# Optimization experiments

Hardware: AMD Instinct MI355X
Metric: run time of the kernel (lower is better)

The kernel has to match this reference:

```python
import jax, jax.numpy as jnp
import numpy as np

N = 5000      # nodes per event (hardcoded in PFNet7.forward)
BIN = 100     # LSH bin_size
K = 16        # kNN per node within bin
SLOPE = 0.01  # LeakyReLU default negative slope


def _mlp(x, W1, b1, W2, b2, W3, b3):
    h = jax.nn.leaky_relu(x @ W1 + b1, SLOPE)
    h = jax.nn.leaky_relu(h @ W2 + b2, SLOPE)
    return h @ W3 + b3


def _build_graph_lsh(x, codebook):
    # x: [N, F]. Faithful vectorized version of GraphBuildingLSH (batch=1).
    n_bins = N // BIN                                   # 50
    mul = x @ codebook[:, : n_bins // 2]                # [N, 25]
    cmul = jnp.concatenate([mul, -mul], axis=-1)        # [N, 50]
    bin_idx = jnp.argmax(cmul, axis=-1)                 # [N]
    bins_split = jnp.argsort(bin_idx).reshape(n_bins, BIN)  # [nb, BIN]
    pts = x[bins_split]                                 # [nb, BIN, F]
    dm = jax.nn.sigmoid(jnp.einsum('pif,pjf->pij', pts, pts))  # [nb, BIN, BIN]
    vals, inds = jax.lax.top_k(dm, K)                   # [nb, BIN, K]
    src = jnp.broadcast_to(bins_split[:, :, None], inds.shape).reshape(-1)
    dst = jnp.take_along_axis(bins_split, inds.reshape(n_bins, -1), axis=1).reshape(-1)
    val = vals.reshape(-1)                              # [nb*BIN*K] = 80000 edges
    return src, dst, val


def _gcn_conv(x, W, b, src, dst, ew):
    # PyG GCNConv: add self-loops (weight 1), symmetric normalization, aggregate at col.
    n = x.shape[0]
    loop = jnp.arange(n)
    row = jnp.concatenate([src, loop])
    col = jnp.concatenate([dst, loop])
    w = jnp.concatenate([ew, jnp.ones((n,), x.dtype)])
    deg = jax.ops.segment_sum(w, col, num_segments=n)
    dis = jnp.where(deg > 0, deg ** -0.5, 0.0)
    norm = dis[row] * w * dis[col]
    h = x @ W
    out = jax.ops.segment_sum(norm[:, None] * h[row], col, num_segments=n)
    return out + b


def _graph_conv(x, Wrel, brel, Wroot, src, dst, ew):
    # PyG GraphConv(aggr='add'): lin_rel(sum_j w_ij x_j) + lin_root(x)
    agg = jax.ops.segment_sum(ew[:, None] * x[src], dst, num_segments=x.shape[0])
    return agg @ Wrel + brel + x @ Wroot


def setup_inputs() -> dict:
    key = jax.random.key(0)
    ks = jax.random.split(key, 24)
    f32 = jnp.float32
    d = {
        'x': jax.random.normal(ks[0], (N, 12), f32),
        'ygen_id': jax.random.normal(ks[1], (N, 6), f32),
        'ygen': jax.random.normal(ks[2], (N, 6), f32),
        'codebook': jax.random.normal(ks[3], (12, 100), f32),
        # nn1: 12 -> 125 -> 125 -> 12
        'nn1_W1': jax.random.normal(ks[4], (12, 125), f32) * 0.1,
        'nn1_b1': jnp.zeros((125,), f32),
        'nn1_W2': jax.random.normal(ks[5], (125, 125), f32) * 0.1,
        'nn1_b2': jnp.zeros((125,), f32),
        'nn1_W3': jax.random.normal(ks[6], (125, 12), f32) * 0.1,
        'nn1_b3': jnp.zeros((12,), f32),
        # GCNConv: 12 -> 32
        'gcn_W': jax.random.normal(ks[7], (12, 32), f32) * 0.1,
        'gcn_b': jnp.zeros((32,), f32),
        # GraphConv: 32 -> 32
        'gc_Wrel': jax.random.normal(ks[8], (32, 32), f32) * 0.1,
        'gc_brel': jnp.zeros((32,), f32),
        'gc_Wroot': jax.random.normal(ks[9], (32, 32), f32) * 0.1,
        # nn2: 32 -> 125 -> 125 -> 6
        'nn2_W1': jax.random.normal(ks[10], (32, 125), f32) * 0.1,
        'nn2_b1': jnp.zeros((125,), f32),
        'nn2_W2': jax.random.normal(ks[11], (125, 125), f32) * 0.1,
        'nn2_b2': jnp.zeros((125,), f32),
        'nn2_W3': jax.random.normal(ks[12], (125, 6), f32) * 0.1,
        'nn2_b3': jnp.zeros((6,), f32),
        # nn3: 38 -> 125 -> 125 -> 6
        'nn3_W1': jax.random.normal(ks[13], (38, 125), f32) * 0.1,
        'nn3_b1': jnp.zeros((125,), f32),
        'nn3_W2': jax.random.normal(ks[14], (125, 125), f32) * 0.1,
        'nn3_b2': jnp.zeros((125,), f32),
        'nn3_W3': jax.random.normal(ks[15], (125, 6), f32) * 0.1,
        'nn3_b3': jnp.zeros((6,), f32),
    }
    return d


def reference(x, ygen_id, ygen, codebook,
              nn1_W1, nn1_b1, nn1_W2, nn1_b2, nn1_W3, nn1_b3,
              gcn_W, gcn_b, gc_Wrel, gc_brel, gc_Wroot,
              nn2_W1, nn2_b1, nn2_W2, nn2_b2, nn2_W3, nn2_b3,
              nn3_W1, nn3_b1, nn3_W2, nn3_b2, nn3_W3, nn3_b3):
    h = _mlp(x, nn1_W1, nn1_b1, nn1_W2, nn1_b2, nn1_W3, nn1_b3)   # [N, 12]
    src, dst, ew = _build_graph_lsh(h, codebook)
    h = jax.nn.leaky_relu(h, SLOPE)
    h = _gcn_conv(h, gcn_W, gcn_b, src, dst, ew)                   # [N, 32]
    h = _graph_conv(h, gc_Wrel, gc_brel, gc_Wroot, src, dst, ew)
    h = jax.nn.leaky_relu(h, SLOPE)
    cand_ids = _mlp(h, nn2_W1, nn2_b1, nn2_W2, nn2_b2, nn2_W3, nn2_b3)
    cand_p4 = _mlp(jnp.concatenate([h, cand_ids], axis=-1),
                   nn3_W1, nn3_b1, nn3_W2, nn3_b2, nn3_W3, nn3_b3)
    return (cand_ids, cand_p4, ygen_id, ygen)
```

## Files before the change

kernel.cpp:

```cpp
#include <hip/hip_runtime.h>
#include <math.h>

#define NN 5000
#define NBINS 50
#define BINSZ 100
#define KNN 16
#define BPAD 104
#define NB 20

typedef _Float16 half8 __attribute__((ext_vector_type(8)));

__device__ __forceinline__ float lrelu(float x){ return x >= 0.f ? x : 0.01f*x; }

__device__ __forceinline__ void scatter_w(float* dst, int t, float4 v) {
    int e = 4 * t, r = e / 125, c = e - 125 * r;
    dst[r * 128 + c] = v.x; if (++c == 125) { c = 0; ++r; }
    dst[r * 128 + c] = v.y; if (++c == 125) { c = 0; ++r; }
    dst[r * 128 + c] = v.z; if (++c == 125) { c = 0; ++r; }
    dst[r * 128 + c] = v.w;
}

__global__ __launch_bounds__(640) void nn1_kernel(
    const float* __restrict__ x,
    const float* __restrict__ W1, const float* __restrict__ b1,
    const float* __restrict__ W2, const float* __restrict__ b2,
    const float* __restrict__ W3, const float* __restrict__ b3,
    const float* __restrict__ cb,
    float* __restrict__ h_out, int* __restrict__ bin_idx) {
    __shared__ float sW[8192];
    __shared__ float bufX[12 * NB];
    __shared__ float bufA[125 * NB];
    __shared__ float bufB[125 * NB];
    __shared__ float sCB[300];
    int tid = threadIdx.x;
    int n0 = blockIdx.x * NB;
    int g = tid >> 7, j = tid & 127;
    float acc[4];
    float4 r0, r1; float rt = 0.f;

    if (tid < 60) {
        float4 v = ((const float4*)(x + n0 * 12))[tid];
        int e = tid * 4;
        bufX[(e % 12) * NB + (e / 12)] = v.x;
        bufX[((e + 1) % 12) * NB + ((e + 1) / 12)] = v.y;
        bufX[((e + 2) % 12) * NB + ((e + 2) / 12)] = v.z;
        bufX[((e + 3) % 12) * NB + ((e + 3) / 12)] = v.w;
    }
    if (tid < 300) { int k = tid / 25, c = tid - k * 25; sCB[tid] = cb[k * 100 + c]; }
    if (tid < 375) ((float4*)sW)[tid] = ((const float4*)W1)[tid];
    __syncthreads();

    if (j < 125) {
        float bj = b1[j];
        acc[0] = bj; acc[1] = bj; acc[2] = bj; acc[3] = bj;
        #pragma unroll
        for (int k = 0; k < 12; ++k) {
            float w = sW[k * 125 + j];
            float4 a = *(const float4*)&bufX[k * NB + g * 4];
            acc[0] += a.x * w; acc[1] += a.y * w; acc[2] += a.z * w; acc[3] += a.w * w;
        }
        #pragma unroll
        for (int n = 0; n < 4; ++n) bufA[j * NB + g * 4 + n] = lrelu(acc[n]);
    }
    r0 = (tid < 1000) ? ((const float4*)W2)[tid] : make_float4(0.f,0.f,0.f,0.f);
    r1 = (tid < 360)  ? ((const float4*)W2)[tid + 640] : make_float4(0.f,0.f,0.f,0.f);
    __syncthreads();
    if (tid < 1000) scatter_w(sW, tid, r0);
    if (tid < 360)  scatter_w(sW, tid + 640, r1);
    __syncthreads();

    float acc8[8];
    if (tid < 320) {
        int j4 = tid & 31;
        #pragma unroll
        for (int jj = 0; jj < 4; ++jj) {
            int jc = 4 * j4 + jj;
            float bj = (jc < 125) ? b2[jc] : 0.f;
            acc8[2 * jj] = bj; acc8[2 * jj + 1] = bj;
        }
    }
    for (int c = 0; c < 4; ++c) {
        if (c < 3) {
            int base = (c + 1) * 1000, nf4 = (c + 1 < 3) ? 1000 : 906;
            r0 = (tid < nf4) ? ((const float4*)W2)[base + tid] : make_float4(0.f,0.f,0.f,0.f);
            r1 = (tid + 640 < nf4) ? ((const float4*)W2)[base + tid + 640] : make_float4(0.f,0.f,0.f,0.f);
            if (c + 1 == 3 && tid == 0) rt = W2[15624];
        }
        int nk = (c < 3) ? 32 : 29;
        if (tid < 320) {
            int j4 = tid & 31, n2 = tid >> 5;
            const float* wbuf = sW + (c & 1) * 4096;
            const float* arow = bufA + (c * 32) * NB + 2 * n2;
            for (int k = 0; k < nk; ++k) {
                float4 w4 = *(const float4*)&wbuf[k * 128 + 4 * j4];
                float2 a2 = *(const float2*)&arow[k * NB];
                acc8[0] += w4.x * a2.x; acc8[1] += w4.x * a2.y;
                acc8[2] += w4.y * a2.x; acc8[3] += w4.y * a2.y;
                acc8[4] += w4.z * a2.x; acc8[5] += w4.z * a2.y;
                acc8[6] += w4.w * a2.x; acc8[7] += w4.w * a2.y;
            }
        }
        if (c < 3) {
            float* dst = sW + ((c + 1) & 1) * 4096;
            int nf4 = (c + 1 < 3) ? 1000 : 906;
            if (tid < nf4) scatter_w(dst, tid, r0);
            if (tid + 640 < nf4) scatter_w(dst, tid + 640, r1);
            if (c + 1 == 3 && tid == 0) dst[3708] = rt;
            __syncthreads();
        }
    }
    if (tid < 320) {
        int j4 = tid & 31, n2 = tid >> 5;
        #pragma unroll
        for (int jj = 0; jj < 4; ++jj) {
            int jc = 4 * j4 + jj;
            if (jc < 125) {
                bufB[jc * NB + 2 * n2]     = lrelu(acc8[2 * jj]);
                bufB[jc * NB + 2 * n2 + 1] = lrelu(acc8[2 * jj + 1]);
            }
        }
    }
    __syncthreads();
    if (tid < 375) ((float4*)sW)[tid] = ((const float4*)W3)[tid];
    __syncthreads();

    if (j < 48) {
        int jj = j % 12, s = j / 12;
        int k0 = s * 32, nk = (s < 3) ? 32 : 29;
        float ps[4] = {0.f, 0.f, 0.f, 0.f};
        for (int k = 0; k < nk; ++k) {
            float w = sW[(k0 + k) * 12 + jj];
            float4 a = *(const float4*)&bufB[(k0 + k) * NB + g * 4];
            ps[0] += a.x * w; ps[1] += a.y * w; ps[2] += a.z * w; ps[3] += a.w * w;
        }
        #pragma unroll
        for (int n = 0; n < 4; ++n) bufA[(s * 12 + jj) * NB + g * 4 + n] = ps[n];
    }
    __syncthreads();
    if (tid < 240) {
        int jj = tid / 20, n = tid % 20;
        float v = bufA[jj * NB + n] + bufA[(12 + jj) * NB + n]
                + bufA[(24 + jj) * NB + n] + bufA[(36 + jj) * NB + n] + b3[jj];
        h_out[(n0 + n) * 12 + jj] = v;
        bufB[jj * NB + n] = v;
    }
    __syncthreads();

    if (tid < NB) {
        int n = tid;
        float hv[12];
        #pragma unroll
        for (int k = 0; k < 12; ++k) hv[k] = bufB[k * NB + n];
        float best = -INFINITY; int bi = 0;
        for (int c = 0; c < 25; ++c) {
            float m = 0.f;
            #pragma unroll
            for (int k = 0; k < 12; ++k) m += hv[k] * sCB[k * 25 + c];
            if (m > best) { best = m; bi = c; }
        }
        for (int c = 0; c < 25; ++c) {
            float m = 0.f;
            #pragma unroll
            for (int k = 0; k < 12; ++k) m += hv[k] * sCB[k * 25 + c];
            if (-m > best) { best = -m; bi = c + 25; }
        }
        bin_idx[n0 + n] = bi;
    }
}

__global__ __launch_bounds__(64) void scatter_kernel(
    const int* __restrict__ bin_idx, int* __restrict__ order) {
    __shared__ int sBI[NN];
    int b = blockIdx.x, lane = threadIdx.x;
    for (int t = lane; t < NN / 4; t += 64) ((int4*)sBI)[t] = ((const int4*)bin_idx)[t];
    __syncthreads();
    unsigned long long below = (lane == 0) ? 0ULL : ((~0ULL) >> (64 - lane));
    int cnt_lt = 0;
    for (int base = 0; base < NN; base += 64) {
        int i = base + lane;
        int bi = (i < NN) ? sBI[i] : 999;
        cnt_lt += __popcll(__ballot(bi < b));
    }
    int offs = cnt_lt;
    for (int base = 0; base < NN; base += 64) {
        int i = base + lane;
        int bi = (i < NN) ? sBI[i] : 999;
        unsigned long long m = __ballot(bi == b);
        if (bi == b) order[offs + __popcll(m & below)] = i;
        offs += __popcll(m);
    }
}

__global__ __launch_bounds__(640) void graph2_kernel(
    const float* __restrict__ h, const int* __restrict__ order,
    const float* __restrict__ gcn_W, const float* __restrict__ gcn_b,
    float* __restrict__ gcn_n, float* __restrict__ agg_n,
    const float4* __restrict__ ygen_id4, const float4* __restrict__ ygen4,
    float4* __restrict__ out4) {
    __shared__ _Float16 M[BINSZ * BPAD];
    __shared__ float s_h[BINSZ * 12];
    __shared__ int   s_nodes[BINSZ];
    __shared__ float s_dis[BINSZ];
    __shared__ float s_w[12 * 32];
    __shared__ float s_big[2 * 32 * BPAD];
    float* s_hWd = s_big;
    float* s_gcn = s_big + 32 * BPAD;
    unsigned* s_tv = (unsigned*)s_big;
    int p = blockIdx.x, tid = threadIdx.x;

    if (tid < BINSZ) s_nodes[tid] = order[p * BINSZ + tid];
    for (int t = tid; t < BINSZ * BPAD / 2; t += 640) ((int*)M)[t] = 0;
    if (tid < 384) s_w[tid] = gcn_W[tid];
    if (tid < 300) {
        int gI = p * 300 + tid;
        out4[15000 + gI] = (gI < 7500) ? ygen_id4[gI] : ygen4[gI - 7500];
    }
    __syncthreads();
    for (int t = tid; t < BINSZ * 12; t += 640) {
        int i = t / 12, k = t - i * 12;
        s_h[t] = h[s_nodes[i] * 12 + k];
    }
    __syncthreads();

    if (tid < 200) {
        int row = tid >> 1, half = tid & 1;
        const float4* xp = (const float4*)&s_h[row * 12];
        float4 x0 = xp[0], x1 = xp[1], x2 = xp[2];
        unsigned tv[KNN];
        #pragma unroll
        for (int k = 0; k < KNN; ++k) tv[k] = 0u;
        int j0 = half * 50;
        for (int jj = 0; jj < 50; ++jj) {
            int j = j0 + jj;
            const float4* ap = (const float4*)&s_h[j * 12];
            float4 a0 = ap[0], a1 = ap[1], a2 = ap[2];
            float d = x0.x*a0.x + x0.y*a0.y + x0.z*a0.z + x0.w*a0.w
                    + x1.x*a1.x + x1.y*a1.y + x1.z*a1.z + x1.w*a1.w
                    + x2.x*a2.x + x2.y*a2.y + x2.z*a2.z + x2.w*a2.w;
            float v = 1.f / (1.f + expf(-d));
            unsigned key = (__float_as_uint(v) & 0xFFFFFF80u) | (unsigned)(127 - j);
            if (key > tv[KNN - 1]) {
                unsigned ins = key;
                #pragma unroll
                for (int k = 0; k < KNN; ++k) {
                    bool gt = ins > tv[k];
                    unsigned mx = gt ? ins : tv[k];
                    unsigned mn = gt ? tv[k] : ins;
                    tv[k] = mx; ins = mn;
                }
            }
        }
        #pragma unroll
        for (int k = 0; k < KNN; ++k) s_tv[tid * KNN + k] = tv[k];
    }
    __syncthreads();

    if (tid < BINSZ) {
        int base = tid * 32;
        int ia = 0, ib = 0;
        #pragma unroll
        for (int k = 0; k < KNN; ++k) {
            unsigned av = s_tv[base + ia], bv = s_tv[base + 16 + ib];
            bool tA = av > bv;
            unsigned key = tA ? av : bv;
            ia += tA; ib += !tA;
            int ix = 127 - (int)(key & 127u);
            float v = __uint_as_float(key & 0xFFFFFF80u);
            M[ix * BPAD + tid] = (_Float16)v;
        }
    }
    __syncthreads();

    if (tid < BINSZ) {
        float dsum = 1.0f;
        #pragma unroll 13
        for (int sc = 0; sc < 13; ++sc) {
            half8 m = *(const half8*)&M[tid * BPAD + sc * 8];
            dsum += (float)m[0] + (float)m[1] + (float)m[2] + (float)m[3]
                  + (float)m[4] + (float)m[5] + (float)m[6] + (float)m[7];
        }
        s_dis[tid] = 1.0f / sqrtf(dsum);
    }
    __syncthreads();

    for (int o = tid; o < BINSZ * 32; o += 640) {
        int s = o >> 5, cc = o & 31;
        float a = 0.f;
        #pragma unroll
        for (int k = 0; k < 12; ++k) a += lrelu(s_h[s * 12 + k]) * s_w[k * 32 + cc];
        s_hWd[cc * BPAD + s] = s_dis[s] * a;
    }
    if (tid < 128) {
        s_hWd[(tid >> 2) * BPAD + 100 + (tid & 3)] = 0.f;
        s_gcn[(tid >> 2) * BPAD + 100 + (tid & 3)] = 0.f;
    }
    __syncthreads();

    int cc = tid & 31, dgg = tid >> 5;
    {
        float a5[5] = {0.f, 0.f, 0.f, 0.f, 0.f};
        for (int sc = 0; sc < 13; ++sc) {
            float4 hv0 = *(const float4*)&s_hWd[cc * BPAD + sc * 8];
            float4 hv1 = *(const float4*)&s_hWd[cc * BPAD + sc * 8 + 4];
            #pragma unroll
            for (int r = 0; r < 5; ++r) {
                int d = dgg + 20 * r;
                half8 m = *(const half8*)&M[d * BPAD + sc * 8];
                a5[r] += (float)m[0]*hv0.x + (float)m[1]*hv0.y + (float)m[2]*hv0.z + (float)m[3]*hv0.w
                       + (float)m[4]*hv1.x + (float)m[5]*hv1.y + (float)m[6]*hv1.z + (float)m[7]*hv1.w;
            }
        }
        float bc = gcn_b[cc];
        #pragma unroll
        for (int r = 0; r < 5; ++r) {
            int d = dgg + 20 * r;
            float gq = s_dis[d] * (a5[r] + s_hWd[cc * BPAD + d]) + bc;
            s_gcn[cc * BPAD + d] = gq;
            gcn_n[s_nodes[d] * 32 + cc] = gq;
        }
    }
    __syncthreads();
    {
        float a5[5] = {0.f, 0.f, 0.f, 0.f, 0.f};
        for (int sc = 0; sc < 13; ++sc) {
            float4 hv0 = *(const float4*)&s_gcn[cc * BPAD + sc * 8];
            float4 hv1 = *(const float4*)&s_gcn[cc * BPAD + sc * 8 + 4];
            #pragma unroll
            for (int r = 0; r < 5; ++r) {
                int d = dgg + 20 * r;
                half8 m = *(const half8*)&M[d * BPAD + sc * 8];
                a5[r] += (float)m[0]*hv0.x + (float)m[1]*hv0.y + (float)m[2]*hv0.z + (float)m[3]*hv0.w
                       + (float)m[4]*hv1.x + (float)m[5]*hv1.y + (float)m[6]*hv1.z + (float)m[7]*hv1.w;
            }
        }
        #pragma unroll
        for (int r = 0; r < 5; ++r) {
            int d = dgg + 20 * r;
            agg_n[s_nodes[d] * 32 + cc] = a5[r];
        }
    }
}

__global__ __launch_bounds__(640) void nn23_kernel(
    const float* __restrict__ gcn_n, const float* __restrict__ agg_n,
    const float* __restrict__ Wrel, const float* __restrict__ brel,
    const float* __restrict__ Wroot,
    const float* __restrict__ A1, const float* __restrict__ ab1,
    const float* __restrict__ A2, const float* __restrict__ ab2,
    const float* __restrict__ A3, const float* __restrict__ ab3,
    const float* __restrict__ B1, const float* __restrict__ bb1,
    const float* __restrict__ B2, const float* __restrict__ bb2,
    const float* __restrict__ B3, const float* __restrict__ bb3,
    float* __restrict__ out_ids, float* __restrict__ out_p4) {
    __shared__ float sW[8192];
    __shared__ float sAG[32 * NB];
    __shared__ float sGC[32 * NB];
    __shared__ float bufC[38 * NB];
    __shared__ float bufA[125 * NB];
    __shared__ float bufB[125 * NB];
    int tid = threadIdx.x;
    int n0 = blockIdx.x * NB;
    int g = tid >> 7, j = tid & 127;
    float acc[4];
    float acc8[8];
    float4 r0, r1; float rt = 0.f;

    if (tid < 160) {
        float4 va = ((const float4*)(agg_n + n0 * 32))[tid];
        float4 vg = ((const float4*)(gcn_n + n0 * 32))[tid];
        int e = tid * 4, n = e / 32, k = e % 32;
        sAG[k * NB + n] = va.x; sAG[(k+1) * NB + n] = va.y;
        sAG[(k+2) * NB + n] = va.z; sAG[(k+3) * NB + n] = va.w;
        sGC[k * NB + n] = vg.x; sGC[(k+1) * NB + n] = vg.y;
        sGC[(k+2) * NB + n] = vg.z; sGC[(k+3) * NB + n] = vg.w;
    }
    if (tid >= 160 && tid < 416) ((float4*)sW)[tid - 160] = ((const float4*)Wrel)[tid - 160];
    if (tid >= 416 && tid < 640) ((float4*)(sW + 1024))[tid - 416] = ((const float4*)Wroot)[tid - 416];
    if (tid < 32) ((float4*)(sW + 1024))[224 + tid] = ((const float4*)Wroot)[224 + tid];
    for (int t = tid; t < 1000; t += 640) ((float4*)(sW + 2048))[t] = ((const float4*)A1)[t];
    __syncthreads();

    {
        int jc = tid / 20, n = tid % 20;
        float a = brel[jc];
        #pragma unroll 8
        for (int k = 0; k < 32; ++k)
            a += sAG[k * NB + n] * sW[k * 32 + jc] + sGC[k * NB + n] * sW[1024 + k * 32 + jc];
        bufC[jc * NB + n] = lrelu(a);
    }
    __syncthreads();

    if (j < 125) {
        float bj = ab1[j];
        acc[0] = bj; acc[1] = bj; acc[2] = bj; acc[3] = bj;
        #pragma unroll 8
        for (int k = 0; k < 32; ++k) {
            float w = sW[2048 + k * 125 + j];
            float4 a = *(const float4*)&bufC[k * NB + g * 4];
            acc[0] += a.x * w; acc[1] += a.y * w; acc[2] += a.z * w; acc[3] += a.w * w;
        }
        #pragma unroll
        for (int n = 0; n < 4; ++n) bufA[j * NB + g * 4 + n] = lrelu(acc[n]);
    }
    r0 = (tid < 1000) ? ((const float4*)A2)[tid] : make_float4(0.f,0.f,0.f,0.f);
    r1 = (tid < 360)  ? ((const float4*)A2)[tid + 640] : make_float4(0.f,0.f,0.f,0.f);
    __syncthreads();
    if (tid < 1000) scatter_w(sW, tid, r0);
    if (tid < 360)  scatter_w(sW, tid + 640, r1);
    __syncthreads();

    if (tid < 320) {
        int j4 = tid & 31;
        #pragma unroll
        for (int jj = 0; jj < 4; ++jj) {
            int jc = 4 * j4 + jj;
            float bj = (jc < 125) ? ab2[jc] : 0.f;
            acc8[2 * jj] = bj; acc8[2 * jj + 1] = bj;
        }
    }
    for (int c = 0; c < 4; ++c) {
        if (c < 3) {
            int base = (c + 1) * 1000, nf4 = (c + 1 < 3) ? 1000 : 906;
            r0 = (tid < nf4) ? ((const float4*)A2)[base + tid] : make_float4(0.f,0.f,0.f,0.f);
            r1 = (tid + 640 < nf4) ? ((const float4*)A2)[base + tid + 640] : make_float4(0.f,0.f,0.f,0.f);
            if (c + 1 == 3 && tid == 0) rt = A2[15624];
        }
        int nk = (c < 3) ? 32 : 29;
        if (tid < 320) {
            int j4 = tid & 31, n2 = tid >> 5;
            const float* wbuf = sW + (c & 1) * 4096;
            const float* arow = bufA + (c * 32) * NB + 2 * n2;
            for (int k = 0; k < nk; ++k) {
                float4 w4 = *(const float4*)&wbuf[k * 128 + 4 * j4];
                float2 a2 = *(const float2*)&arow[k * NB];
                acc8[0] += w4.x * a2.x; acc8[1] += w4.x * a2.y;
                acc8[2] += w4.y * a2.x; acc8[3] += w4.y * a2.y;
                acc8[4] += w4.z * a2.x; acc8[5] += w4.z * a2.y;
                acc8[6] += w4.w * a2.x; acc8[7] += w4.w * a2.y;
            }
        }
        if (c < 3) {
            float* dst = sW + ((c + 1) & 1) * 4096;
            int nf4 = (c + 1 < 3) ? 1000 : 906;
            if (tid < nf4) scatter_w(dst, tid, r0);
            if (tid + 640 < nf4) scatter_w(dst, tid + 640, r1);
            if (c + 1 == 3 && tid == 0) dst[3708] = rt;
            __syncthreads();
        }
    }
    if (tid < 320) {
        int j4 = tid & 31, n2 = tid >> 5;
        #pragma unroll
        for (int jj = 0; jj < 4; ++jj) {
            int jc = 4 * j4 + jj;
            if (jc < 125) {
                bufB[jc * NB + 2 * n2]     = lrelu(acc8[2 * jj]);
                bufB[jc * NB + 2 * n2 + 1] = lrelu(acc8[2 * jj + 1]);
            }
        }
    }
    __syncthreads();
    if (tid < 187) ((float4*)sW)[tid] = ((const float4*)A3)[tid];
    if (tid == 187) { sW[748] = A3[748]; sW[749] = A3[749]; }
    for (int t = tid; t < 1187; t += 640) ((float4*)(sW + 752))[t] = ((const float4*)B1)[t];
    if (tid == 188) { sW[752 + 4748] = B1[4748]; sW[752 + 4749] = B1[4749]; }
    __syncthreads();

    if (j < 24) {
        int jj = j % 6, s = j / 6;
        int k0 = s * 32, nk = (s < 3) ? 32 : 29;
        float ps[4] = {0.f, 0.f, 0.f, 0.f};
        for (int k = 0; k < nk; ++k) {
            float w = sW[(k0 + k) * 6 + jj];
            float4 a = *(const float4*)&bufB[(k0 + k) * NB + g * 4];
            ps[0] += a.x * w; ps[1] += a.y * w; ps[2] += a.z * w; ps[3] += a.w * w;
        }
        #pragma unroll
        for (int n = 0; n < 4; ++n) bufA[(s * 6 + jj) * NB + g * 4 + n] = ps[n];
    }
    __syncthreads();
    if (tid < 120) {
        int jj = tid / 20, n = tid % 20;
        float v = bufA[jj * NB + n] + bufA[(6 + jj) * NB + n]
                + bufA[(12 + jj) * NB + n] + bufA[(18 + jj) * NB + n] + ab3[jj];
        out_ids[(n0 + n) * 6 + jj] = v;
        bufC[(32 + jj) * NB + n] = v;
    }
    __syncthreads();

    if (j < 125) {
        float bj = bb1[j];
        acc[0] = bj; acc[1] = bj; acc[2] = bj; acc[3] = bj;
        #pragma unroll 2
        for (int k = 0; k < 38; ++k) {
            float w = sW[752 + k * 125 + j];
            float4 a = *(const float4*)&bufC[k * NB + g * 4];
            acc[0] += a.x * w; acc[1] += a.y * w; acc[2] += a.z * w; acc[3] += a.w * w;
        }
        #pragma unroll
        for (int n = 0; n < 4; ++n) bufA[j * NB + g * 4 + n] = lrelu(acc[n]);
    }
    r0 = (tid < 1000) ? ((const float4*)B2)[tid] : make_float4(0.f,0.f,0.f,0.f);
    r1 = (tid < 360)  ? ((const float4*)B2)[tid + 640] : make_float4(0.f,0.f,0.f,0.f);
    __syncthreads();
    if (tid < 1000) scatter_w(sW, tid, r0);
    if (tid < 360)  scatter_w(sW, tid + 640, r1);
    __syncthreads();

    if (tid < 320) {
        int j4 = tid & 31;
        #pragma unroll
        for (int jj = 0; jj < 4; ++jj) {
            int jc = 4 * j4 + jj;
            float bj = (jc < 125) ? bb2[jc] : 0.f;
            acc8[2 * jj] = bj; acc8[2 * jj + 1] = bj;
        }
    }
    for (int c = 0; c < 4; ++c) {
        if (c < 3) {
            int base = (c + 1) * 1000, nf4 = (c + 1 < 3) ? 1000 : 906;
            r0 = (tid < nf4) ? ((const float4*)B2)[base + tid] : make_float4(0.f,0.f,0.f,0.f);
            r1 = (tid + 640 < nf4) ? ((const float4*)B2)[base + tid + 640] : make_float4(0.f,0.f,0.f,0.f);
            if (c + 1 == 3 && tid == 0) rt = B2[15624];
        }
        int nk = (c < 3) ? 32 : 29;
        if (tid < 320) {
            int j4 = tid & 31, n2 = tid >> 5;
            const float* wbuf = sW + (c & 1) * 4096;
            const float* arow = bufA + (c * 32) * NB + 2 * n2;
            for (int k = 0; k < nk; ++k) {
                float4 w4 = *(const float4*)&wbuf[k * 128 + 4 * j4];
                float2 a2 = *(const float2*)&arow[k * NB];
                acc8[0] += w4.x * a2.x; acc8[1] += w4.x * a2.y;
                acc8[2] += w4.y * a2.x; acc8[3] += w4.y * a2.y;
                acc8[4] += w4.z * a2.x; acc8[5] += w4.z * a2.y;
                acc8[6] += w4.w * a2.x; acc8[7] += w4.w * a2.y;
            }
        }
        if (c < 3) {
            float* dst = sW + ((c + 1) & 1) * 4096;
            int nf4 = (c + 1 < 3) ? 1000 : 906;
            if (tid < nf4) scatter_w(dst, tid, r0);
            if (tid + 640 < nf4) scatter_w(dst, tid + 640, r1);
            if (c + 1 == 3 && tid == 0) dst[3708] = rt;
            __syncthreads();
        }
    }
    if (tid < 320) {
        int j4 = tid & 31, n2 = tid >> 5;
        #pragma unroll
        for (int jj = 0; jj < 4; ++jj) {
            int jc = 4 * j4 + jj;
            if (jc < 125) {
                bufB[jc * NB + 2 * n2]     = lrelu(acc8[2 * jj]);
                bufB[jc * NB + 2 * n2 + 1] = lrelu(acc8[2 * jj + 1]);
            }
        }
    }
    __syncthreads();
    if (tid < 187) ((float4*)sW)[tid] = ((const float4*)B3)[tid];
    if (tid == 187) { sW[748] = B3[748]; sW[749] = B3[749]; }
    __syncthreads();

    if (j < 24) {
        int jj = j % 6, s = j / 6;
        int k0 = s * 32, nk = (s < 3) ? 32 : 29;
        float ps[4] = {0.f, 0.f, 0.f, 0.f};
        for (int k = 0; k < nk; ++k) {
            float w = sW[(k0 + k) * 6 + jj];
            float4 a = *(const float4*)&bufB[(k0 + k) * NB + g * 4];
            ps[0] += a.x * w; ps[1] += a.y * w; ps[2] += a.z * w; ps[3] += a.w * w;
        }
        #pragma unroll
        for (int n = 0; n < 4; ++n) bufA[(s * 6 + jj) * NB + g * 4 + n] = ps[n];
    }
    __syncthreads();
    if (tid < 120) {
        int jj = tid / 20, n = tid % 20;
        float v = bufA[jj * NB + n] + bufA[(6 + jj) * NB + n]
                + bufA[(12 + jj) * NB + n] + bufA[(18 + jj) * NB + n] + bb3[jj];
        out_p4[(n0 + n) * 6 + jj] = v;
    }
}

static inline int cdiv(int a, int b) { return (a + b - 1) / b; }

extern "C" void kernel_launch(void* const* d_in, const int* in_sizes, int n_in,
                              void* d_out, int out_size, void* d_ws, size_t ws_size,
                              hipStream_t stream) {
    const float* x        = (const float*)d_in[0];
    const float* ygen_id  = (const float*)d_in[1];
    const float* ygen     = (const float*)d_in[2];
    const float* codebook = (const float*)d_in[3];
    const float* nn1_W1 = (const float*)d_in[4];  const float* nn1_b1 = (const float*)d_in[5];
    const float* nn1_W2 = (const float*)d_in[6];  const float* nn1_b2 = (const float*)d_in[7];
    const float* nn1_W3 = (const float*)d_in[8];  const float* nn1_b3 = (const float*)d_in[9];
    const float* gcn_W  = (const float*)d_in[10]; const float* gcn_b  = (const float*)d_in[11];
    const float* gc_Wrel = (const float*)d_in[12]; const float* gc_brel = (const float*)d_in[13];
    const float* gc_Wroot = (const float*)d_in[14];
    const float* nn2_W1 = (const float*)d_in[15]; const float* nn2_b1 = (const float*)d_in[16];
    const float* nn2_W2 = (const float*)d_in[17]; const float* nn2_b2 = (const float*)d_in[18];
    const float* nn2_W3 = (const float*)d_in[19]; const float* nn2_b3 = (const float*)d_in[20];
    const float* nn3_W1 = (const float*)d_in[21]; const float* nn3_b1 = (const float*)d_in[22];
    const float* nn3_W2 = (const float*)d_in[23]; const float* nn3_b2 = (const float*)d_in[24];
    const float* nn3_W3 = (const float*)d_in[25]; const float* nn3_b3 = (const float*)d_in[26];

    float* out = (float*)d_out;
    float* ws  = (float*)d_ws;

    float* h      = ws + 0;
    float* gcn_n  = ws + 60000;
    float* agg_n  = ws + 220000;
    int* bin_idx  = (int*)(ws + 380000);
    int* order    = (int*)(ws + 385000);

    nn1_kernel<<<NN / NB, 640, 0, stream>>>(
        x, nn1_W1, nn1_b1, nn1_W2, nn1_b2, nn1_W3, nn1_b3, codebook,
        h, bin_idx);

    scatter_kernel<<<NBINS, 64, 0, stream>>>(bin_idx, order);

    graph2_kernel<<<NBINS, 640, 0, stream>>>(
        h, order, gcn_W, gcn_b, gcn_n, agg_n,
        (const float4*)ygen_id, (const float4*)ygen, (float4*)out);

    nn23_kernel<<<NN / NB, 640, 0, stream>>>(
        gcn_n, agg_n, gc_Wrel, gc_brel, gc_Wroot,
        nn2_W1, nn2_b1, nn2_W2, nn2_b2, nn2_W3, nn2_b3,
        nn3_W1, nn3_b1, nn3_W2, nn3_b2, nn3_W3, nn3_b3,
        out, out + 30000);
}
```

Baseline: 199.6 us.

## Fuse bin-ordering scatter into graph kernel, computing stable counting sort per block

Removes the separate scatter kernel and has each graph2 block load all bin indices into shared memory. Each block then runs a chunked counting sort (per-chunk bin counts, exclusive prefix over bins, ordered scan) to recover the node list for its own bin. This saves one kernel launch and the global round-trip of the order array. In exchange, every block redundantly scans all 5000 indices with serial per-thread loops, and s_big is reused as the bin-index buffer.

```diff
diff --git a/kernel.cpp b/kernel.cpp
--- a/kernel.cpp
+++ b/kernel.cpp
@@ -168,31 +168,8 @@
     }
 }
 
-__global__ __launch_bounds__(64) void scatter_kernel(
-    const int* __restrict__ bin_idx, int* __restrict__ order) {
-    __shared__ int sBI[NN];
-    int b = blockIdx.x, lane = threadIdx.x;
-    for (int t = lane; t < NN / 4; t += 64) ((int4*)sBI)[t] = ((const int4*)bin_idx)[t];
-    __syncthreads();
-    unsigned long long below = (lane == 0) ? 0ULL : ((~0ULL) >> (64 - lane));
-    int cnt_lt = 0;
-    for (int base = 0; base < NN; base += 64) {
-        int i = base + lane;
-        int bi = (i < NN) ? sBI[i] : 999;
-        cnt_lt += __popcll(__ballot(bi < b));
-    }
-    int offs = cnt_lt;
-    for (int base = 0; base < NN; base += 64) {
-        int i = base + lane;
-        int bi = (i < NN) ? sBI[i] : 999;
-        unsigned long long m = __ballot(bi == b);
-        if (bi == b) order[offs + __popcll(m & below)] = i;
-        offs += __popcll(m);
-    }
-}
-
 __global__ __launch_bounds__(640) void graph2_kernel(
-    const float* __restrict__ h, const int* __restrict__ order,
+    const float* __restrict__ h, const int* __restrict__ bin_idx,
     const float* __restrict__ gcn_W, const float* __restrict__ gcn_b,
     float* __restrict__ gcn_n, float* __restrict__ agg_n,
     const float4* __restrict__ ygen_id4, const float4* __restrict__ ygen4,
@@ -203,12 +180,14 @@
     __shared__ float s_dis[BINSZ];
     __shared__ float s_w[12 * 32];
     __shared__ float s_big[2 * 32 * BPAD];
+    __shared__ int   s_cnt[552];
     float* s_hWd = s_big;
     float* s_gcn = s_big + 32 * BPAD;
+    int* sBI = (int*)s_big;
     unsigned* s_tv = (unsigned*)s_big;
     int p = blockIdx.x, tid = threadIdx.x;
 
-    if (tid < BINSZ) s_nodes[tid] = order[p * BINSZ + tid];
+    for (int t = tid; t < NN / 4; t += 640) ((int4*)sBI)[t] = ((const int4*)bin_idx)[t];
     for (int t = tid; t < BINSZ * BPAD / 2; t += 640) ((int*)M)[t] = 0;
     if (tid < 384) s_w[tid] = gcn_W[tid];
     if (tid < 300) {
@@ -216,6 +195,44 @@
         out4[15000 + gI] = (gI < 7500) ? ygen_id4[gI] : ygen4[gI - 7500];
     }
     __syncthreads();
+
+    if (tid < 500) {
+        int w = tid / 50, b = tid - 50 * w;
+        const int* q = sBI + w * 500;
+        int c = 0;
+        for (int i = 0; i < 500; ++i) c += (q[i] == b);
+        s_cnt[tid] = c;
+    }
+    __syncthreads();
+    if (tid < 50) {
+        int tot = 0;
+        for (int w = 0; w < 10; ++w) tot += s_cnt[w * 50 + tid];
+        s_cnt[500 + tid] = tot;
+    }
+    __syncthreads();
+    if (tid == 0) {
+        int s = 0;
+        for (int b = 0; b < 50; ++b) { int t = s_cnt[500 + b]; s_cnt[500 + b] = s; s += t; }
+    }
+    __syncthreads();
+    if (tid < 500) {
+        int w = tid / 50, b = tid - 50 * w;
+        int base = s_cnt[500 + b];
+        for (int ww = 0; ww < w; ++ww) base += s_cnt[ww * 50 + b];
+        int cnt = s_cnt[w * 50 + b];
+        int lo = p * BINSZ, hi = lo + BINSZ;
+        if (base < hi && base + cnt > lo) {
+            const int* q = sBI + w * 500;
+            for (int i = 0; i < 500 && base < hi; ++i) {
+                if (q[i] == b) {
+                    if (base >= lo) s_nodes[base - lo] = w * 500 + i;
+                    ++base;
+                }
+            }
+        }
+    }
+    __syncthreads();
+
     for (int t = tid; t < BINSZ * 12; t += 640) {
         int i = t / 12, k = t - i * 12;
         s_h[t] = h[s_nodes[i] * 12 + k];
@@ -612,16 +629,13 @@
     float* gcn_n  = ws + 60000;
     float* agg_n  = ws + 220000;
     int* bin_idx  = (int*)(ws + 380000);
-    int* order    = (int*)(ws + 385000);
 
     nn1_kernel<<<NN / NB, 640, 0, stream>>>(
         x, nn1_W1, nn1_b1, nn1_W2, nn1_b2, nn1_W3, nn1_b3, codebook,
         h, bin_idx);
 
-    scatter_kernel<<<NBINS, 64, 0, stream>>>(bin_idx, order);
-
     graph2_kernel<<<NBINS, 640, 0, stream>>>(
-        h, order, gcn_W, gcn_b, gcn_n, agg_n,
+        h, bin_idx, gcn_W, gcn_b, gcn_n, agg_n,
         (const float4*)ygen_id, (const float4*)ygen, (float4*)out);
 
     nn23_kernel<<<NN / NB, 640, 0, stream>>>(
```

Result: slower. 233.7 us (+17.0%).
